# Kernel tuning notes

Measured on AMD Instinct MI355X. Metric: run time of the kernel, lower is better.

## Reference

```python
import jax, jax.numpy as jnp
import numpy as np

MARGIN = 0.2
EPS = 1e-5
NEG_SENTINEL = -1e9


def _cos_sim(a, b):
    a = a / jnp.linalg.norm(a, axis=-1, keepdims=True)
    b = b / jnp.linalg.norm(b, axis=-1, keepdims=True)
    return a @ b.T  # [B, B]


def _row_losses(sm, labels):
    # sm: [B, B] similarity matrix; one loop body of the original, vectorized over rows i.
    diag = jnp.diagonal(sm)                      # pos_pair_ (scalar per row)
    pos_valid = diag < (1.0 - EPS)               # pos_pair_[pos_pair_ < 1-eps]
    neg_mask = labels[None, :] != labels[:, None]
    # neg_pair_[neg_pair_ + margin > min(pos_pair_)] ; min of a scalar is itself
    hard = neg_mask & ((sm + MARGIN) > diag[:, None])
    has_neg = jnp.any(hard, axis=1)
    neg_max = jnp.max(jnp.where(hard, sm, NEG_SENTINEL), axis=1)  # max(neg_pair)
    valid = pos_valid & has_neg
    pos_loss = jnp.maximum(0.2 * diag * diag - 0.7 * diag + 0.5, 0.0)
    neg_loss = jnp.maximum(0.9 * neg_max * neg_max - 0.4 * neg_max + 0.03, 0.0)
    return jnp.sum(jnp.where(valid, pos_loss + neg_loss, 0.0))


def setup_inputs() -> dict:
    key = jax.random.key(0)
    k1, k2 = jax.random.split(key)
    B, D = 8192, 256
    audio_embeds = jax.random.normal(k1, (B, D), dtype=jnp.float32)
    text_embeds = jax.random.normal(k2, (B, D), dtype=jnp.float32)
    labels = jnp.arange(B, dtype=jnp.int64)
    return {"audio_embeds": audio_embeds, "text_embeds": text_embeds, "labels": labels}


def reference(audio_embeds, text_embeds, labels):
    scores = _cos_sim(audio_embeds, text_embeds)  # [B, B]
    B = scores.shape[0]
    total = _row_losses(scores, labels) + _row_losses(scores.T, labels)
    return total / B
```

## Files before the change

kernel.cpp:

```cpp
#include <hip/hip_runtime.h>
#include <stdint.h>

#define BM 128
#define BN 128
#define KD 256

typedef __attribute__((ext_vector_type(4))) float f32x4;
typedef __attribute__((ext_vector_type(4))) int   i32x4;
typedef __attribute__((ext_vector_type(8))) int   i32x8;

__device__ __forceinline__ float fmax4(f32x4 v) {
  return fmaxf(fmaxf(v[0], v[1]), fmaxf(v[2], v[3]));
}

__global__ __launch_bounds__(256) void norm_kernel(
    const float* __restrict__ a, const float* __restrict__ b,
    unsigned int* __restrict__ an, unsigned int* __restrict__ bn,
    float* __restrict__ diag, float* __restrict__ out, int D) {
  if (blockIdx.x == 0 && threadIdx.x == 0) out[0] = 0.f;
  const int row = blockIdx.x * 4 + (threadIdx.x >> 6);
  const int l = threadIdx.x & 63;
  const float4 av = ((const float4*)(a + (size_t)row * D))[l];
  const float4 bv = ((const float4*)(b + (size_t)row * D))[l];
  float ssa = av.x*av.x + av.y*av.y + av.z*av.z + av.w*av.w;
  float ssb = bv.x*bv.x + bv.y*bv.y + bv.z*bv.z + bv.w*bv.w;
  float dot = av.x*bv.x + av.y*bv.y + av.z*bv.z + av.w*bv.w;
  for (int off = 1; off < 64; off <<= 1) {
    ssa += __shfl_xor(ssa, off, 64);
    ssb += __shfl_xor(ssb, off, 64);
    dot += __shfl_xor(dot, off, 64);
  }
  const float inva = 1.0f / sqrtf(ssa);
  const float invb = 1.0f / sqrtf(ssb);
  if (l == 0) diag[row] = dot * inva * invb;
  int pa = 0, pb = 0;
  pa = __builtin_amdgcn_cvt_pk_fp8_f32(av.x * inva, av.y * inva, pa, 0);
  pa = __builtin_amdgcn_cvt_pk_fp8_f32(av.z * inva, av.w * inva, pa, 1);
  pb = __builtin_amdgcn_cvt_pk_fp8_f32(bv.x * invb, bv.y * invb, pb, 0);
  pb = __builtin_amdgcn_cvt_pk_fp8_f32(bv.z * invb, bv.w * invb, pb, 1);
  an[(size_t)row * (D / 4) + l] = (unsigned int)pa;
  bn[(size_t)row * (D / 4) + l] = (unsigned int)pb;
}

__global__ __launch_bounds__(256, 4) void gemm_max_kernel(
    const unsigned char* __restrict__ an, const unsigned char* __restrict__ bn,
    const int* __restrict__ labels,
    float* __restrict__ row_part, float* __restrict__ col_part, int B) {
  __shared__ __align__(16) unsigned char sA[BM * 128];
  __shared__ __align__(16) unsigned char sB[BN * 128];
  __shared__ float lds_col[2][BN];

  const int tid  = threadIdx.x;
  const int lane = tid & 63;
  const int w    = tid >> 6;
  const int wm   = w >> 1, wn = w & 1;
  const int tj   = blockIdx.x & 63;
  const int ti   = blockIdx.x >> 6;

  const int sr  = lane >> 3;
  const int sc8 = lane & 7;
  const int ssw = (sc8 ^ sr) * 16;

  const int fr = lane & 15;
  const int hi = lane >> 4;
  const int p0 = ((2 * hi)     ^ (fr & 7)) * 16;
  const int p1 = ((2 * hi + 1) ^ (fr & 7)) * 16;

  f32x4 acc[4][4];
  #pragma unroll
  for (int mt = 0; mt < 4; ++mt)
    #pragma unroll
    for (int nt = 0; nt < 4; ++nt)
      acc[mt][nt] = (f32x4){0.f, 0.f, 0.f, 0.f};

  const int SC = 0x7F7F7F7F;

  #pragma unroll
  for (int it = 0; it < 2; ++it) {
    #pragma unroll
    for (int c = 0; c < 4; ++c) {
      const int r0 = w * 32 + c * 8;
      const unsigned char* ga = an + (size_t)(ti * BM + r0 + sr) * KD + it * 128 + ssw;
      const unsigned char* gb = bn + (size_t)(tj * BN + r0 + sr) * KD + it * 128 + ssw;
      __builtin_amdgcn_global_load_lds(
          (const __attribute__((address_space(1))) void*)ga,
          (__attribute__((address_space(3))) void*)(sA + r0 * 128 + lane * 16), 16, 0, 0);
      __builtin_amdgcn_global_load_lds(
          (const __attribute__((address_space(1))) void*)gb,
          (__attribute__((address_space(3))) void*)(sB + r0 * 128 + lane * 16), 16, 0, 0);
    }
    __syncthreads();

    i32x8 bf[4];
    #pragma unroll
    for (int nt = 0; nt < 4; ++nt) {
      const unsigned char* rb = sB + (wn * 64 + nt * 16 + fr) * 128;
      i32x4 blo = *(const i32x4*)(rb + p0), bhi = *(const i32x4*)(rb + p1);
      bf[nt] = __builtin_shufflevector(blo, bhi, 0, 1, 2, 3, 4, 5, 6, 7);
    }
    #pragma unroll
    for (int mt = 0; mt < 4; ++mt) {
      const unsigned char* ra = sA + (wm * 64 + mt * 16 + fr) * 128;
      i32x4 alo = *(const i32x4*)(ra + p0), ahi = *(const i32x4*)(ra + p1);
      i32x8 af = __builtin_shufflevector(alo, ahi, 0, 1, 2, 3, 4, 5, 6, 7);
      #pragma unroll
      for (int nt = 0; nt < 4; ++nt)
        acc[mt][nt] = __builtin_amdgcn_mfma_scale_f32_16x16x128_f8f6f4(
            af, bf[nt], acc[mt][nt], 0, 0, 0, SC, 0, SC);
    }
    __syncthreads();
  }

  int li[4][4], labc[4];
  #pragma unroll
  for (int mt = 0; mt < 4; ++mt)
    #pragma unroll
    for (int r = 0; r < 4; ++r)
      li[mt][r] = labels[ti * BM + wm * 64 + mt * 16 + hi * 4 + r];
  #pragma unroll
  for (int nt = 0; nt < 4; ++nt)
    labc[nt] = labels[tj * BN + wn * 64 + nt * 16 + fr];

  float rp[4][4];
  float cp[4] = {-1e9f, -1e9f, -1e9f, -1e9f};
  #pragma unroll
  for (int mt = 0; mt < 4; ++mt)
    #pragma unroll
    for (int r = 0; r < 4; ++r) {
      const int l0 = li[mt][r];
      float rm = -1e9f;
      #pragma unroll
      for (int nt = 0; nt < 4; ++nt) {
        const float vm = (l0 != labc[nt]) ? acc[mt][nt][r] : -1e9f;
        rm = fmaxf(rm, vm);
        cp[nt] = fmaxf(cp[nt], vm);
      }
      rp[mt][r] = rm;
    }

  float* red = (float*)sA;
  const int s = wn * 16 + fr;
  #pragma unroll
  for (int mt = 0; mt < 4; ++mt)
    #pragma unroll
    for (int r = 0; r < 4; ++r) {
      const int i = wm * 64 + mt * 16 + hi * 4 + r;
      red[i * 32 + (((s >> 2) ^ (i & 7)) << 2) + (s & 3)] = rp[mt][r];
    }

  #pragma unroll
  for (int nt = 0; nt < 4; ++nt) {
    float c = cp[nt];
    c = fmaxf(c, __shfl_xor(c, 16, 64));
    c = fmaxf(c, __shfl_xor(c, 32, 64));
    if (hi == 0) lds_col[wm][wn * 64 + nt * 16 + fr] = c;
  }
  __syncthreads();

  if (tid < BM) {
    const int key = tid & 7;
    const f32x4* rr = (const f32x4*)(red + tid * 32);
    f32x4 m4 = rr[0 ^ key];
    #pragma unroll
    for (int k = 1; k < 8; ++k) {
      f32x4 v = rr[k ^ key];
      m4[0] = fmaxf(m4[0], v[0]); m4[1] = fmaxf(m4[1], v[1]);
      m4[2] = fmaxf(m4[2], v[2]); m4[3] = fmaxf(m4[3], v[3]);
    }
    row_part[(size_t)tj * B + ti * BM + tid] = fmax4(m4);
  } else if (tid < BM + BN) {
    const int t2 = tid - BM;
    col_part[(size_t)ti * B + tj * BN + t2] =
        fmaxf(lds_col[0][t2], lds_col[1][t2]);
  }
}

__global__ __launch_bounds__(256) void finalize_kernel(
    const float* __restrict__ row_part, const float* __restrict__ col_part,
    const float* __restrict__ diag, int B, int T, float* __restrict__ out) {
  const int v = blockIdx.x * 256 + threadIdx.x;
  const bool isrow = v < B;
  const int i = isrow ? v : v - B;
  const float* part = isrow ? row_part : col_part;
  float m = -1e9f;
  for (int t = 0; t < T; ++t) m = fmaxf(m, part[(size_t)t * B + i]);
  const float d = diag[i];
  float loss = 0.f;
  if ((d < 1.0f - 1e-5f) && (m + 0.2f > d)) {
    loss = fmaxf(0.2f * d * d - 0.7f * d + 0.5f, 0.f) +
           fmaxf(0.9f * m * m - 0.4f * m + 0.03f, 0.f);
  }
  for (int off = 1; off < 64; off <<= 1) loss += __shfl_xor(loss, off, 64);
  __shared__ float ssum[4];
  if ((threadIdx.x & 63) == 0) ssum[threadIdx.x >> 6] = loss;
  __syncthreads();
  if (threadIdx.x == 0)
    atomicAdd(out, (ssum[0] + ssum[1] + ssum[2] + ssum[3]) / (float)B);
}

extern "C" void kernel_launch(void* const* d_in, const int* in_sizes, int n_in,
                              void* d_out, int out_size, void* d_ws, size_t ws_size,
                              hipStream_t stream) {
  const float* a      = (const float*)d_in[0];
  const float* b      = (const float*)d_in[1];
  const int*   labels = (const int*)d_in[2];
  const int B = in_sizes[2];
  const int D = in_sizes[0] / B;
  const int T = B / BM;

  char* ws = (char*)d_ws;
  unsigned char* an = (unsigned char*)ws;
  unsigned char* bn = (unsigned char*)(ws + (size_t)B * D);
  float* diag     = (float*)(ws + (size_t)2 * B * D);
  float* row_part = diag + B;
  float* col_part = row_part + (size_t)T * B;

  norm_kernel<<<B / 4, 256, 0, stream>>>(a, b, (unsigned int*)an,
                                         (unsigned int*)bn, diag,
                                         (float*)d_out, D);

  gemm_max_kernel<<<(B / BM) * (B / BN), 256, 0, stream>>>(
      an, bn, labels, row_part, col_part, B);

  finalize_kernel<<<(2 * B) / 256, 256, 0, stream>>>(
      row_part, col_part, diag, B, T, (float*)d_out);
}
```

Baseline: 121.5 us.

## Load FP8 MFMA operands directly from global memory, bypassing LDS staging

```diff
diff --git a/kernel.cpp b/kernel.cpp
--- a/kernel.cpp
+++ b/kernel.cpp
@@ -42,12 +42,11 @@
   bn[(size_t)row * (D / 4) + l] = (unsigned int)pb;
 }
 
-__global__ __launch_bounds__(256, 4) void gemm_max_kernel(
+__global__ __launch_bounds__(256) void gemm_max_kernel(
     const unsigned char* __restrict__ an, const unsigned char* __restrict__ bn,
     const int* __restrict__ labels,
     float* __restrict__ row_part, float* __restrict__ col_part, int B) {
-  __shared__ __align__(16) unsigned char sA[BM * 128];
-  __shared__ __align__(16) unsigned char sB[BN * 128];
+  __shared__ __align__(16) float red[BM * 32];
   __shared__ float lds_col[2][BN];
 
   const int tid  = threadIdx.x;
@@ -57,14 +56,11 @@
   const int tj   = blockIdx.x & 63;
   const int ti   = blockIdx.x >> 6;
 
-  const int sr  = lane >> 3;
-  const int sc8 = lane & 7;
-  const int ssw = (sc8 ^ sr) * 16;
-
   const int fr = lane & 15;
   const int hi = lane >> 4;
-  const int p0 = ((2 * hi)     ^ (fr & 7)) * 16;
-  const int p1 = ((2 * hi + 1) ^ (fr & 7)) * 16;
+
+  const unsigned char* Ab = an + (size_t)(ti * BM + wm * 64 + fr) * KD + hi * 32;
+  const unsigned char* Bb = bn + (size_t)(tj * BN + wn * 64 + fr) * KD + hi * 32;
 
   f32x4 acc[4][4];
   #pragma unroll
@@ -77,38 +73,25 @@
 
   #pragma unroll
   for (int it = 0; it < 2; ++it) {
-    #pragma unroll
-    for (int c = 0; c < 4; ++c) {
-      const int r0 = w * 32 + c * 8;
-      const unsigned char* ga = an + (size_t)(ti * BM + r0 + sr) * KD + it * 128 + ssw;
-      const unsigned char* gb = bn + (size_t)(tj * BN + r0 + sr) * KD + it * 128 + ssw;
-      __builtin_amdgcn_global_load_lds(
-          (const __attribute__((address_space(1))) void*)ga,
-          (__attribute__((address_space(3))) void*)(sA + r0 * 128 + lane * 16), 16, 0, 0);
-      __builtin_amdgcn_global_load_lds(
-          (const __attribute__((address_space(1))) void*)gb,
-          (__attribute__((address_space(3))) void*)(sB + r0 * 128 + lane * 16), 16, 0, 0);
-    }
-    __syncthreads();
-
     i32x8 bf[4];
     #pragma unroll
     for (int nt = 0; nt < 4; ++nt) {
-      const unsigned char* rb = sB + (wn * 64 + nt * 16 + fr) * 128;
-      i32x4 blo = *(const i32x4*)(rb + p0), bhi = *(const i32x4*)(rb + p1);
-      bf[nt] = __builtin_shufflevector(blo, bhi, 0, 1, 2, 3, 4, 5, 6, 7);
+      const unsigned char* rb = Bb + (size_t)(nt * 16) * KD + it * 128;
+      bf[nt] = __builtin_shufflevector(*(const i32x4*)rb,
+                                       *(const i32x4*)(rb + 16),
+                                       0, 1, 2, 3, 4, 5, 6, 7);
     }
     #pragma unroll
     for (int mt = 0; mt < 4; ++mt) {
-      const unsigned char* ra = sA + (wm * 64 + mt * 16 + fr) * 128;
-      i32x4 alo = *(const i32x4*)(ra + p0), ahi = *(const i32x4*)(ra + p1);
-      i32x8 af = __builtin_shufflevector(alo, ahi, 0, 1, 2, 3, 4, 5, 6, 7);
+      const unsigned char* ra = Ab + (size_t)(mt * 16) * KD + it * 128;
+      i32x8 af = __builtin_shufflevector(*(const i32x4*)ra,
+                                         *(const i32x4*)(ra + 16),
+                                         0, 1, 2, 3, 4, 5, 6, 7);
       #pragma unroll
       for (int nt = 0; nt < 4; ++nt)
         acc[mt][nt] = __builtin_amdgcn_mfma_scale_f32_16x16x128_f8f6f4(
             af, bf[nt], acc[mt][nt], 0, 0, 0, SC, 0, SC);
     }
-    __syncthreads();
   }
 
   int li[4][4], labc[4];
@@ -138,7 +121,6 @@
       rp[mt][r] = rm;
     }
 
-  float* red = (float*)sA;
   const int s = wn * 16 + fr;
   #pragma unroll
   for (int mt = 0; mt < 4; ++mt)
```

After: 151.3 us. 24.5% more time.
